# Performance work log

Hardware: AMD Instinct MI355X
Metric: run time of the kernel (lower is better)

Reference implementation:

```python
import jax, jax.numpy as jnp
import numpy as np

N = 50000   # nodes
E = 800000  # edges (avg degree 16)
F_IN = 128
H = 128
L = 4
LN_EPS = 1e-5


def setup_inputs() -> dict:
    key = jax.random.key(0)
    ks = jax.random.split(key, 4)
    x = jax.random.normal(ks[0], (N, F_IN), dtype=jnp.float32)
    edge_index = jax.random.randint(ks[1], (2, E), 0, N)
    conv_w = jax.random.normal(ks[2], (L, F_IN, H), dtype=jnp.float32) * 0.05
    conv_b = jnp.zeros((L, H), dtype=jnp.float32)
    ln_g = jnp.ones((L, H), dtype=jnp.float32)
    ln_b = jnp.zeros((L, H), dtype=jnp.float32)
    head_w = jax.random.normal(ks[3], (H, 1), dtype=jnp.float32) * 0.05
    head_b = jnp.zeros((1,), dtype=jnp.float32)
    return {"x": x, "edge_index": edge_index, "conv_w": conv_w, "conv_b": conv_b,
            "ln_g": ln_g, "ln_b": ln_b, "head_w": head_w, "head_b": head_b}


def _layer_norm(h, g, b):
    mu = jnp.mean(h, axis=-1, keepdims=True)
    var = jnp.mean(jnp.square(h - mu), axis=-1, keepdims=True)
    return (h - mu) * jax.lax.rsqrt(var + LN_EPS) * g + b


def _gcn_conv(h, W, b, src, dst, inv_sqrt_deg, inv_deg):
    # PyG GCNConv: self-loops + symmetric normalization D^-1/2 (A+I) D^-1/2, then bias.
    hw = h @ W  # (N, H)
    norm = inv_sqrt_deg[src] * inv_sqrt_deg[dst]  # (E,)
    msg = hw[src] * norm[:, None]  # gather + edgewise scale
    agg = jax.ops.segment_sum(msg, dst, num_segments=N)  # scatter-add
    agg = agg + hw * inv_deg[:, None]  # self-loop term (norm = 1/deg)
    return agg + b


def reference(x, edge_index, conv_w, conv_b, ln_g, ln_b, head_w, head_b):
    src, dst = edge_index[0], edge_index[1]
    # degree on target nodes, including self-loop
    deg = jax.ops.segment_sum(jnp.ones((E,), x.dtype), dst, num_segments=N) + 1.0
    inv_sqrt_deg = jax.lax.rsqrt(deg)
    inv_deg = 1.0 / deg
    h = x
    for i in range(L):
        h = _gcn_conv(h, conv_w[i], conv_b[i], src, dst, inv_sqrt_deg, inv_deg)
        h = _layer_norm(h, ln_g[i], ln_b[i])
        if i != L - 1:
            h = jax.nn.gelu(h, approximate=False)
            # dropout is identity in eval mode
    scores = (h @ head_w + head_b).squeeze(-1)  # (N,)
    return scores, h
```

## Files before the change

kernel.cpp:

```cpp
#include <hip/hip_runtime.h>
#include <math.h>

#define N_NODES 50000
#define N_EDGES 800000
#define HDIM 128
#define NLAYERS 4
#define LN_EPS 1e-5f
#define EQUARTER (N_EDGES / 4)
#define SEG 64

typedef __attribute__((ext_vector_type(8))) short short8;
typedef __attribute__((ext_vector_type(4))) float floatx4;

__device__ __forceinline__ ushort f2bf(float x) {
    unsigned b = __float_as_uint(x);
    unsigned r = b + 0x7fffu + ((b >> 16) & 1u);
    return (ushort)(r >> 16);
}
__device__ __forceinline__ float2 bf2f2(unsigned u) {
    return make_float2(__uint_as_float(u << 16), __uint_as_float(u & 0xffff0000u));
}


__global__ void fill_kernel(const int* __restrict__ src, const int* __restrict__ dst,
                            int* __restrict__ cnt, ushort* __restrict__ csr16) {
    int t = blockIdx.x * blockDim.x + threadIdx.x;
    if (t >= EQUARTER) return;
    int s0 = src[t],                d0 = dst[t];
    int s1 = src[t + EQUARTER],     d1 = dst[t + EQUARTER];
    int s2 = src[t + 2 * EQUARTER], d2 = dst[t + 2 * EQUARTER];
    int s3 = src[t + 3 * EQUARTER], d3 = dst[t + 3 * EQUARTER];
    int p0 = atomicAdd(&cnt[d0], 1);
    int p1 = atomicAdd(&cnt[d1], 1);
    int p2 = atomicAdd(&cnt[d2], 1);
    int p3 = atomicAdd(&cnt[d3], 1);
    if (p0 < SEG) csr16[d0 * SEG + p0] = (ushort)s0;
    if (p1 < SEG) csr16[d1 * SEG + p1] = (ushort)s1;
    if (p2 < SEG) csr16[d2 * SEG + p2] = (ushort)s2;
    if (p3 < SEG) csr16[d3 * SEG + p3] = (ushort)s3;
}

__global__ __launch_bounds__(256) void isd_kernel(const int* __restrict__ cnt,
                                                  float* __restrict__ isd,
                                                  float* __restrict__ ind) {
    int i = blockIdx.x * 256 + threadIdx.x;
    if (i < N_NODES) {
        float d = (float)cnt[i] + 1.0f;
        isd[i] = rsqrtf(d);
        ind[i] = 1.0f / d;
    }
}

__global__ __launch_bounds__(256) void bprep_kernel(const float* __restrict__ W,
                                                    ushort* __restrict__ bfrag) {
    int idx = blockIdx.x * 256 + threadIdx.x;
    if (idx >= NLAYERS * 4 * 8 * 64) return;
    int lane = idx & 63;
    int t = (idx >> 6) & 7;
    int s = (idx >> 9) & 3;
    int l = idx >> 11;
    int n = t * 16 + (lane & 15);
    int kb = s * 32 + (lane >> 4) * 8;
    const float* Wl = W + (size_t)l * HDIM * HDIM;
    union { uint4 q; ushort u[8]; } o;
#pragma unroll
    for (int j = 0; j < 8; ++j) o.u[j] = f2bf(Wl[(size_t)(kb + j) * HDIM + n]);
    *(uint4*)&bfrag[(size_t)idx * 8] = o.q;
}

template <bool A_FP32>
__global__ __launch_bounds__(256) void gemm_mfma_kernel(const void* __restrict__ Av,
                                                        const ushort* __restrict__ bfrag,
                                                        ushort* __restrict__ out) {
    int wave = threadIdx.x >> 6, lane = threadIdx.x & 63;
    int quad = lane >> 4, mrow = lane & 15;
    int rowBase = blockIdx.x * 64 + wave * 16;
    int arow = rowBase + mrow;
    bool aok = arow < N_NODES;

    floatx4 acc[8];
#pragma unroll
    for (int t = 0; t < 8; ++t) acc[t] = (floatx4)0.f;

#pragma unroll
    for (int s = 0; s < 4; ++s) {
        union { short8 v; ushort u[8]; } af;
        if (A_FP32) {
            const float* A = (const float*)Av;
            if (aok) {
                const float* p = &A[(size_t)arow * HDIM + s * 32 + quad * 8];
#pragma unroll
                for (int j = 0; j < 8; ++j) af.u[j] = f2bf(p[j]);
            } else {
#pragma unroll
                for (int j = 0; j < 8; ++j) af.u[j] = 0;
            }
        } else {
            const ushort* A = (const ushort*)Av;
            if (aok) {
                af.v = *(const short8*)&A[(size_t)arow * HDIM + s * 32 + quad * 8];
            } else {
#pragma unroll
                for (int j = 0; j < 8; ++j) af.u[j] = 0;
            }
        }
#pragma unroll
        for (int t = 0; t < 8; ++t) {
            short8 bf = *(const short8*)&bfrag[(size_t)(((s * 8 + t) * 64) + lane) * 8];
            acc[t] = __builtin_amdgcn_mfma_f32_16x16x32_bf16(af.v, bf, acc[t], 0, 0, 0);
        }
    }
#pragma unroll
    for (int t = 0; t < 8; ++t) {
#pragma unroll
        for (int r = 0; r < 4; ++r) {
            int row = rowBase + quad * 4 + r;
            if (row < N_NODES) out[(size_t)row * HDIM + t * 16 + mrow] = f2bf(acc[t][r]);
        }
    }
}

__global__ __launch_bounds__(256) void agg_ln_kernel(
    const unsigned* __restrict__ hwu, const int* __restrict__ degcnt,
    const ushort* __restrict__ csr16, const float* __restrict__ isd,
    const float* __restrict__ ind, const float* __restrict__ conv_b,
    const float* __restrict__ ln_g, const float* __restrict__ ln_b,
    unsigned* __restrict__ hout_bf, float* __restrict__ hout_f32,
    const float* __restrict__ head_w, const float* __restrict__ head_b,
    float* __restrict__ scores, int final_layer) {
    int wave = threadIdx.x >> 6;
    int lane = threadIdx.x & 63;
    int n = blockIdx.x * 4 + wave;
    if (n >= N_NODES) return;
    int c = lane * 2;

    float2 hv = bf2f2(hwu[(size_t)n * 64 + lane]);
    float isd_n = isd[n];
    float ind_n = ind[n];
    int rs = n * SEG;
    int deg = min(degcnt[n], SEG);

    float ex = 0.f, ey = 0.f;
    {
        int m = deg;
        int sj = 0;
        float wj = 0.f;
        if (lane < m) {
            sj = (int)csr16[rs + lane];
            wj = isd[sj];
        }
        for (int j = 0; j < m; j += 8) {
            int s0 = __shfl(sj, j + 0), s1 = __shfl(sj, j + 1);
            int s2 = __shfl(sj, j + 2), s3 = __shfl(sj, j + 3);
            int s4 = __shfl(sj, j + 4), s5 = __shfl(sj, j + 5);
            int s6 = __shfl(sj, j + 6), s7 = __shfl(sj, j + 7);
            float w0 = __shfl(wj, j + 0), w1 = __shfl(wj, j + 1);
            float w2 = __shfl(wj, j + 2), w3 = __shfl(wj, j + 3);
            float w4 = __shfl(wj, j + 4), w5 = __shfl(wj, j + 5);
            float w6 = __shfl(wj, j + 6), w7 = __shfl(wj, j + 7);
            unsigned u0 = hwu[(size_t)s0 * 64 + lane];
            unsigned u1 = hwu[(size_t)s1 * 64 + lane];
            unsigned u2 = hwu[(size_t)s2 * 64 + lane];
            unsigned u3 = hwu[(size_t)s3 * 64 + lane];
            unsigned u4 = hwu[(size_t)s4 * 64 + lane];
            unsigned u5 = hwu[(size_t)s5 * 64 + lane];
            unsigned u6 = hwu[(size_t)s6 * 64 + lane];
            unsigned u7 = hwu[(size_t)s7 * 64 + lane];
            float2 v0 = bf2f2(u0), v1 = bf2f2(u1), v2 = bf2f2(u2), v3 = bf2f2(u3);
            float2 v4 = bf2f2(u4), v5 = bf2f2(u5), v6 = bf2f2(u6), v7 = bf2f2(u7);
            ex = fmaf(v0.x, w0, ex); ey = fmaf(v0.y, w0, ey);
            ex = fmaf(v1.x, w1, ex); ey = fmaf(v1.y, w1, ey);
            ex = fmaf(v2.x, w2, ex); ey = fmaf(v2.y, w2, ey);
            ex = fmaf(v3.x, w3, ex); ey = fmaf(v3.y, w3, ey);
            ex = fmaf(v4.x, w4, ex); ey = fmaf(v4.y, w4, ey);
            ex = fmaf(v5.x, w5, ex); ey = fmaf(v5.y, w5, ey);
            ex = fmaf(v6.x, w6, ex); ey = fmaf(v6.y, w6, ey);
            ex = fmaf(v7.x, w7, ex); ey = fmaf(v7.y, w7, ey);
        }
    }
    float2 cb = *(const float2*)&conv_b[c];
    float ax = fmaf(ex, isd_n, fmaf(hv.x, ind_n, cb.x));
    float ay = fmaf(ey, isd_n, fmaf(hv.y, ind_n, cb.y));

    float sum = ax + ay;
#pragma unroll
    for (int o = 32; o; o >>= 1) sum += __shfl_xor(sum, o);
    float mu = sum * (1.0f / HDIM);
    float dx = ax - mu, dy = ay - mu;
    float vs = dx * dx + dy * dy;
#pragma unroll
    for (int o = 32; o; o >>= 1) vs += __shfl_xor(vs, o);
    float rstd = rsqrtf(vs * (1.0f / HDIM) + LN_EPS);
    float2 g = *(const float2*)&ln_g[c];
    float2 b = *(const float2*)&ln_b[c];
    float yx = fmaf(dx * rstd, g.x, b.x);
    float yy = fmaf(dy * rstd, g.y, b.y);

    if (!final_layer) {
        yx = 0.5f * yx * (1.0f + erff(yx * 0.70710678118654752f));
        yy = 0.5f * yy * (1.0f + erff(yy * 0.70710678118654752f));
        hout_bf[(size_t)n * 64 + lane] = (unsigned)f2bf(yx) | ((unsigned)f2bf(yy) << 16);
    } else {
        *(float2*)&hout_f32[(size_t)n * HDIM + c] = make_float2(yx, yy);
        float2 hwv = *(const float2*)&head_w[c];
        float p = yx * hwv.x + yy * hwv.y;
#pragma unroll
        for (int o = 32; o; o >>= 1) p += __shfl_xor(p, o);
        if (lane == 0) scores[n] = p + head_b[0];
    }
}


extern "C" void kernel_launch(void* const* d_in, const int* in_sizes, int n_in,
                              void* d_out, int out_size, void* d_ws, size_t ws_size,
                              hipStream_t stream) {
    const float* x      = (const float*)d_in[0];
    const int*   eidx   = (const int*)d_in[1];
    const float* conv_w = (const float*)d_in[2];
    const float* conv_b = (const float*)d_in[3];
    const float* ln_g   = (const float*)d_in[4];
    const float* ln_b   = (const float*)d_in[5];
    const float* head_w = (const float*)d_in[6];
    const float* head_b = (const float*)d_in[7];
    float* out = (float*)d_out;

    const int* src = eidx;
    const int* dst = eidx + N_EDGES;

    char* ws = (char*)d_ws;
    size_t o = 0;
    auto alloc = [&](size_t elems) {
        void* p = ws + o * 4;
        o += (elems + 15) & ~(size_t)15;
        return p;
    };
    int*      cnt      = (int*)alloc(N_NODES);
    float*    isd      = (float*)alloc(N_NODES);
    float*    ind      = (float*)alloc(N_NODES);
    ushort*   csr16    = (ushort*)alloc((size_t)N_NODES * SEG / 2);
    ushort*   bfrag    = (ushort*)alloc(NLAYERS * 4 * 8 * 64 * 8 / 2);
    unsigned* hw       = (unsigned*)alloc((size_t)N_NODES * 64);
    unsigned* hbuf     = (unsigned*)alloc((size_t)N_NODES * 64);

    hipMemsetAsync(cnt, 0, N_NODES * sizeof(int), stream);
    fill_kernel<<<(EQUARTER + 255) / 256, 256, 0, stream>>>(src, dst, cnt, csr16);
    isd_kernel<<<(N_NODES + 255) / 256, 256, 0, stream>>>(cnt, isd, ind);
    bprep_kernel<<<(NLAYERS * 4 * 8 * 64 + 255) / 256, 256, 0, stream>>>(conv_w, bfrag);

    const void* hin = (const void*)x;
    for (int l = 0; l < NLAYERS; ++l) {
        const ushort* bl = bfrag + (size_t)l * 4 * 8 * 64 * 8;
        if (l == 0)
            gemm_mfma_kernel<true><<<(N_NODES + 63) / 64, 256, 0, stream>>>(hin, bl, (ushort*)hw);
        else
            gemm_mfma_kernel<false><<<(N_NODES + 63) / 64, 256, 0, stream>>>(hin, bl, (ushort*)hw);
        int fin = (l == NLAYERS - 1) ? 1 : 0;
        agg_ln_kernel<<<(N_NODES + 3) / 4, 256, 0, stream>>>(
            hw, cnt, csr16, isd, ind,
            conv_b + (size_t)l * HDIM, ln_g + (size_t)l * HDIM, ln_b + (size_t)l * HDIM,
            hbuf, out + N_NODES, head_w, head_b, out, fin);
        hin = (const void*)hbuf;
    }
}
```

Baseline: 353.1 us.

## Build CSR via two-pass bucketed binning in shared memory instead of global atomics

Replaces the per-edge global atomicAdd CSR fill with a two-pass scheme. The first pass bins edges into buckets of 128 destination nodes in LDS and flushes them to global buckets with one atomic per bucket. The second pass builds each 128-node CSR window in LDS and writes it out coalesced, computing degrees and normalization in the same kernel. This is meant to cut scattered global atomics and uncoalesced 2-byte writes. The cost is an extra global intermediate buffer and fixed capacity caps (GCAP, SEG) that could silently drop edges on skewed inputs.

Result: slower. 665.9 us (+88.6%).

```diff
diff --git a/kernel.cpp b/kernel.cpp
--- a/kernel.cpp
+++ b/kernel.cpp
@@ -6,8 +6,11 @@
 #define HDIM 128
 #define NLAYERS 4
 #define LN_EPS 1e-5f
-#define EQUARTER (N_EDGES / 4)
 #define SEG 64
+#define KBUCK 391
+#define BINCAP 32
+#define GCAP 2560
+#define EPB 2048
 
 typedef __attribute__((ext_vector_type(8))) short short8;
 typedef __attribute__((ext_vector_type(4))) float floatx4;
@@ -22,32 +25,75 @@
 }
 
 
-__global__ void fill_kernel(const int* __restrict__ src, const int* __restrict__ dst,
-                            int* __restrict__ cnt, ushort* __restrict__ csr16) {
-    int t = blockIdx.x * blockDim.x + threadIdx.x;
-    if (t >= EQUARTER) return;
-    int s0 = src[t],                d0 = dst[t];
-    int s1 = src[t + EQUARTER],     d1 = dst[t + EQUARTER];
-    int s2 = src[t + 2 * EQUARTER], d2 = dst[t + 2 * EQUARTER];
-    int s3 = src[t + 3 * EQUARTER], d3 = dst[t + 3 * EQUARTER];
-    int p0 = atomicAdd(&cnt[d0], 1);
-    int p1 = atomicAdd(&cnt[d1], 1);
-    int p2 = atomicAdd(&cnt[d2], 1);
-    int p3 = atomicAdd(&cnt[d3], 1);
-    if (p0 < SEG) csr16[d0 * SEG + p0] = (ushort)s0;
-    if (p1 < SEG) csr16[d1 * SEG + p1] = (ushort)s1;
-    if (p2 < SEG) csr16[d2 * SEG + p2] = (ushort)s2;
-    if (p3 < SEG) csr16[d3 * SEG + p3] = (ushort)s3;
-}
-
-__global__ __launch_bounds__(256) void isd_kernel(const int* __restrict__ cnt,
-                                                  float* __restrict__ isd,
-                                                  float* __restrict__ ind) {
-    int i = blockIdx.x * 256 + threadIdx.x;
-    if (i < N_NODES) {
-        float d = (float)cnt[i] + 1.0f;
-        isd[i] = rsqrtf(d);
-        ind[i] = 1.0f / d;
+__global__ __launch_bounds__(256) void binA_kernel(const int* __restrict__ src,
+                                                   const int* __restrict__ dst,
+                                                   int* __restrict__ gcnt,
+                                                   unsigned* __restrict__ gbuck) {
+    __shared__ unsigned bins[KBUCK][BINCAP];
+    __shared__ int bcnt[KBUCK];
+    for (int i = threadIdx.x; i < KBUCK; i += 256) bcnt[i] = 0;
+    __syncthreads();
+    int base = blockIdx.x * EPB;
+#pragma unroll
+    for (int it = 0; it < EPB / 256; ++it) {
+        int e = base + it * 256 + threadIdx.x;
+        if (e < N_EDGES) {
+            int s = src[e], d = dst[e];
+            int bk = d >> 7;
+            unsigned entry = ((unsigned)(d & 127) << 16) | (unsigned)s;
+            int slot = atomicAdd(&bcnt[bk], 1);
+            if (slot < BINCAP) {
+                bins[bk][slot] = entry;
+            } else {
+                int p = atomicAdd(&gcnt[bk], 1);
+                if (p < GCAP) gbuck[(size_t)bk * GCAP + p] = entry;
+            }
+        }
+    }
+    __syncthreads();
+    int wave = threadIdx.x >> 6, lane = threadIdx.x & 63;
+    for (int bk = wave; bk < KBUCK; bk += 4) {
+        int m = min(bcnt[bk], BINCAP);
+        if (m == 0) continue;
+        int p0 = 0;
+        if (lane == 0) p0 = atomicAdd(&gcnt[bk], m);
+        p0 = __shfl(p0, 0);
+        if (lane < m && p0 + lane < GCAP)
+            gbuck[(size_t)bk * GCAP + p0 + lane] = bins[bk][lane];
+    }
+}
+
+__global__ __launch_bounds__(256) void binB_kernel(const int* __restrict__ gcnt,
+                                                   const unsigned* __restrict__ gbuck,
+                                                   ushort* __restrict__ csr16,
+                                                   int* __restrict__ degcnt,
+                                                   float* __restrict__ isd,
+                                                   float* __restrict__ ind) {
+    __shared__ ushort win[128 * SEG];
+    __shared__ int cnt[128];
+    int bk = blockIdx.x;
+    for (int i = threadIdx.x; i < 128; i += 256) cnt[i] = 0;
+    __syncthreads();
+    int M = min(gcnt[bk], GCAP);
+    for (int i = threadIdx.x; i < M; i += 256) {
+        unsigned e = gbuck[(size_t)bk * GCAP + i];
+        int dloc = e >> 16;
+        int slot = atomicAdd(&cnt[dloc], 1);
+        if (slot < SEG) win[dloc * SEG + slot] = (ushort)(e & 0xffffu);
+    }
+    __syncthreads();
+    uint4* wg = (uint4*)win;
+    uint4* outp = (uint4*)(csr16 + (size_t)bk * 128 * SEG);
+    for (int i = threadIdx.x; i < 1024; i += 256) outp[i] = wg[i];
+    for (int i = threadIdx.x; i < 128; i += 256) {
+        int n = bk * 128 + i;
+        if (n < N_NODES) {
+            int dg = cnt[i];
+            degcnt[n] = dg;
+            float d = (float)dg + 1.0f;
+            isd[n] = rsqrtf(d);
+            ind[n] = 1.0f / d;
+        }
     }
 }
 
@@ -234,17 +280,20 @@
         o += (elems + 15) & ~(size_t)15;
         return p;
     };
-    int*      cnt      = (int*)alloc(N_NODES);
+    int*      gcnt     = (int*)alloc(KBUCK);
+    unsigned* gbuck    = (unsigned*)alloc((size_t)KBUCK * GCAP);
+    int*      degcnt   = (int*)alloc(N_NODES);
     float*    isd      = (float*)alloc(N_NODES);
     float*    ind      = (float*)alloc(N_NODES);
-    ushort*   csr16    = (ushort*)alloc((size_t)N_NODES * SEG / 2);
+    ushort*   csr16    = (ushort*)alloc((size_t)KBUCK * 128 * SEG / 2);
     ushort*   bfrag    = (ushort*)alloc(NLAYERS * 4 * 8 * 64 * 8 / 2);
     unsigned* hw       = (unsigned*)alloc((size_t)N_NODES * 64);
     unsigned* hbuf     = (unsigned*)alloc((size_t)N_NODES * 64);
 
-    hipMemsetAsync(cnt, 0, N_NODES * sizeof(int), stream);
-    fill_kernel<<<(EQUARTER + 255) / 256, 256, 0, stream>>>(src, dst, cnt, csr16);
-    isd_kernel<<<(N_NODES + 255) / 256, 256, 0, stream>>>(cnt, isd, ind);
+    hipMemsetAsync(gcnt, 0, KBUCK * sizeof(int), stream);
+    int nA = (N_EDGES + EPB - 1) / EPB;
+    binA_kernel<<<nA, 256, 0, stream>>>(src, dst, gcnt, gbuck);
+    binB_kernel<<<KBUCK, 256, 0, stream>>>(gcnt, gbuck, csr16, degcnt, isd, ind);
     bprep_kernel<<<(NLAYERS * 4 * 8 * 64 + 255) / 256, 256, 0, stream>>>(conv_w, bfrag);
 
     const void* hin = (const void*)x;
@@ -256,7 +305,7 @@
             gemm_mfma_kernel<false><<<(N_NODES + 63) / 64, 256, 0, stream>>>(hin, bl, (ushort*)hw);
         int fin = (l == NLAYERS - 1) ? 1 : 0;
         agg_ln_kernel<<<(N_NODES + 3) / 4, 256, 0, stream>>>(
-            hw, cnt, csr16, isd, ind,
+            hw, degcnt, csr16, isd, ind,
             conv_b + (size_t)l * HDIM, ln_g + (size_t)l * HDIM, ln_b + (size_t)l * HDIM,
             hbuf, out + N_NODES, head_w, head_b, out, fin);
         hin = (const void*)hbuf;
```
